# Performance work log

Measured on AMD Instinct MI355X. Metric: run time of the kernel, lower is better.

## Reference

```python
import jax, jax.numpy as jnp
import numpy as np

K = 20          # neighbors per centroid
OUT_CH = 256    # out_channel
EPS = 1e-5      # batchnorm eps


def _bn(x, gamma, beta, axes):
    # batch-norm in training mode (batch statistics), per-channel on last axis
    mu = jnp.mean(x, axis=axes, keepdims=True)
    var = jnp.var(x, axis=axes, keepdims=True)
    return (x - mu) * jax.lax.rsqrt(var + EPS) * gamma + beta


def _forward(centroid, xyz, radius, dist,
             w_xyz, b_xyz, g0, be0, w1, g1, be1, w2, g2, be2):
    B, N, _ = xyz.shape
    M = centroid.shape[1]
    # --- sample_and_group: radius mask + index sort + gather ---
    ar = jnp.arange(N, dtype=jnp.int32)                       # [N]
    idx = jnp.where(dist > radius, N, ar[None, None, :])      # [B,M,N]
    idx = jnp.sort(idx, axis=-1)[:, :, :K]                    # [B,M,K] lowest in-radius indices
    first = idx[:, :, :1]
    idx = jnp.where(idx == N, first, idx)                     # pad with first neighbor
    pf = jax.vmap(lambda f, i: f[i])(xyz, idx)                # [B,M,K,3] gather
    # --- concat (points, neighbors, variance) -> 9 channels ---
    pts = jnp.broadcast_to(centroid[:, :, None, :], (B, M, K, 3))
    feat = jnp.concatenate([pts, pf, pf - pts], axis=-1)      # [B,M,K,9]
    # --- 1x1 conv2d + BN2d + GELU (exact erf, as torch nn.GELU) ---
    h = jnp.einsum('bmkc,oc->bmko', feat, w_xyz) + b_xyz      # [B,M,K,C/8]
    h = jax.nn.gelu(_bn(h, g0, be0, axes=(0, 1, 2)), approximate=False)
    # --- max over k neighbors ---
    h = jnp.max(h, axis=2)                                    # [B,M,C/8]
    # --- MLP: Conv1x1 (no bias) + BN1d + GELU, then Conv1x1 + BN1d ---
    h = jnp.einsum('bmc,oc->bmo', h, w1)
    h = jax.nn.gelu(_bn(h, g1, be1, axes=(0, 1)), approximate=False)
    h = jnp.einsum('bmc,oc->bmo', h, w2)
    h = _bn(h, g2, be2, axes=(0, 1))                          # [B,M,OUT_CH]
    return h


def setup_inputs() -> dict:
    key = jax.random.key(0)
    ks = jax.random.split(key, 10)
    B, M, N = 4, 2048, 8192
    c8, c4 = OUT_CH // 8, OUT_CH // 4
    return {
        'centroid': jax.random.uniform(ks[0], (B, M, 3), jnp.float32),
        'xyz': jax.random.uniform(ks[1], (B, N, 3), jnp.float32),
        'radius': jax.random.uniform(ks[2], (B, M, 1), jnp.float32),
        'dist': jax.random.uniform(ks[3], (B, M, N), jnp.float32),
        'w_xyz': jax.random.normal(ks[4], (c8, 9), jnp.float32) * 0.3,
        'b_xyz': jnp.zeros((c8,), jnp.float32),
        'g0': jnp.ones((c8,), jnp.float32),
        'be0': jnp.zeros((c8,), jnp.float32),
        'w1': jax.random.normal(ks[5], (c4, c8), jnp.float32) * 0.2,
        'g1': jnp.ones((c4,), jnp.float32),
        'be1': jnp.zeros((c4,), jnp.float32),
        'w2': jax.random.normal(ks[6], (OUT_CH, c4), jnp.float32) * 0.15,
        'g2': jnp.ones((OUT_CH,), jnp.float32),
        'be2': jnp.zeros((OUT_CH,), jnp.float32),
    }


def reference(centroid, xyz, radius, dist, w_xyz, b_xyz, g0, be0,
              w1, g1, be1, w2, g2, be2):
    return _forward(centroid, xyz, radius, dist, w_xyz, b_xyz, g0, be0,
                    w1, g1, be1, w2, g2, be2)
```

## Files before the change

### kernel.cpp

```cpp
#include <hip/hip_runtime.h>
#include <cstdint>
#include <cstddef>

#define K_NB   20
#define N_PTS  8192
#define M_CENT 2048
#define B_SZ   4
#define C8     32
#define C4     64
#define COUT   256
#define EPSV   1e-5f
#define NROWS  (B_SZ * M_CENT)

#define NP0 64
#define NP1 32
#define NP2 16

__device__ __forceinline__ float gelu_exact(float x) {
    return 0.5f * x * (1.0f + erff(x * 0.7071067811865476f));
}

__global__ __launch_bounds__(256) void k_scan_mlp0(
    const float* __restrict__ centroid, const float* __restrict__ xyz,
    const float* __restrict__ radius,   const float* __restrict__ dist,
    const float* __restrict__ w_xyz,    const float* __restrict__ b_xyz,
    float* __restrict__ hmin, float* __restrict__ hmax,
    double* __restrict__ p0sum, double* __restrict__ p0sq)
{
    __shared__ int   idx_sh[4][K_NB];
    __shared__ float ss[256], qq[256];
    const int tid  = threadIdx.x;
    const int wave = tid >> 6;
    const int lane = tid & 63;
    const int row  = blockIdx.x * 4 + wave;
    const int b    = row >> 11;
    const float rad = radius[row];
    const float* drow = dist + (size_t)row * N_PTS;

    int cnt = 0;
    for (int base = 0; base < N_PTS && cnt < K_NB; base += 1024) {
        float4 v[4];
        #pragma unroll
        for (int s = 0; s < 4; s++)
            v[s] = reinterpret_cast<const float4*>(drow + base + s * 256)[lane];
        #pragma unroll
        for (int s = 0; s < 4; s++) {
            unsigned mloc = (v[s].x <= rad ? 1u : 0u) | (v[s].y <= rad ? 2u : 0u)
                          | (v[s].z <= rad ? 4u : 0u) | (v[s].w <= rad ? 8u : 0u);
            uint64_t b0 = __ballot(mloc & 1u);
            uint64_t b1 = __ballot(mloc & 2u);
            uint64_t b2 = __ballot(mloc & 4u);
            uint64_t b3 = __ballot(mloc & 8u);
            uint64_t lt = (1ull << lane) - 1ull;
            int r = __popcll(b0 & lt) + __popcll(b1 & lt)
                  + __popcll(b2 & lt) + __popcll(b3 & lt);
            const int myidx = base + s * 256 + lane * 4;
            if (mloc & 1u) { int p = cnt + r; if (p < K_NB) idx_sh[wave][p] = myidx + 0; r++; }
            if (mloc & 2u) { int p = cnt + r; if (p < K_NB) idx_sh[wave][p] = myidx + 1; r++; }
            if (mloc & 4u) { int p = cnt + r; if (p < K_NB) idx_sh[wave][p] = myidx + 2; r++; }
            if (mloc & 8u) { int p = cnt + r; if (p < K_NB) idx_sh[wave][p] = myidx + 3; r++; }
            cnt += __popcll(b0) + __popcll(b1) + __popcll(b2) + __popcll(b3);
        }
    }
    __syncthreads();

    const int cfill = (cnt < K_NB) ? cnt : K_NB;
    const int fillv = (cnt == 0) ? (N_PTS - 1) : idx_sh[wave][0];
    if (lane < K_NB && lane >= cfill) idx_sh[wave][lane] = fillv;
    __syncthreads();

    const int ch = lane & 31;
    const int kk = lane >> 5;
    const float* w = w_xyz + ch * 9;
    const float wc0 = w[0] - w[6], wc1 = w[1] - w[7], wc2 = w[2] - w[8];
    const float wp0 = w[3] + w[6], wp1 = w[4] + w[7], wp2 = w[5] + w[8];
    const float cterm = b_xyz[ch] + centroid[row * 3 + 0] * wc0
                      + centroid[row * 3 + 1] * wc1
                      + centroid[row * 3 + 2] * wc2;

    float s = 0.f, q = 0.f, mn = 3.0e38f, mx = -3.0e38f;
    #pragma unroll
    for (int t = 0; t < 10; t++) {
        const int idx = idx_sh[wave][2 * t + kk];
        const float* p = xyz + ((size_t)b * N_PTS + idx) * 3;
        const float h = cterm + p[0] * wp0 + p[1] * wp1 + p[2] * wp2;
        s += h; q += h * h;
        mn = fminf(mn, h); mx = fmaxf(mx, h);
    }
    mn = fminf(mn, __shfl_xor(mn, 32));
    mx = fmaxf(mx, __shfl_xor(mx, 32));
    if (lane < 32) hmin[row * C8 + ch] = mn;
    else           hmax[row * C8 + ch] = mx;

    ss[tid] = s; qq[tid] = q;
    __syncthreads();
    if (tid < C8) {
        float S = 0.f, Q = 0.f;
        #pragma unroll
        for (int r = 0; r < 8; r++) { S += ss[tid + 32 * r]; Q += qq[tid + 32 * r]; }
        const int part = blockIdx.x & (NP0 - 1);
        atomicAdd(&p0sum[part * C8 + tid], (double)S);
        atomicAdd(&p0sq [part * C8 + tid], (double)Q);
    }
}

__global__ __launch_bounds__(256) void k_bn0_max_mm1(
    const float* __restrict__ hmin, const float* __restrict__ hmax,
    const double* __restrict__ p0sum, const double* __restrict__ p0sq,
    const float* __restrict__ g0, const float* __restrict__ be0,
    const float* __restrict__ w1, float* __restrict__ h1,
    double* __restrict__ p1sum, double* __restrict__ p1sq)
{
    __shared__ float sc[C8], sh[C8];
    __shared__ float w1s[C4 * C8];
    __shared__ float a_sh[4][C8];
    __shared__ float r1s[4][C4];
    const int tid = threadIdx.x;
    if (tid < C8) {
        double S = 0.0, Q = 0.0;
        #pragma unroll 8
        for (int p = 0; p < NP0; p++) { S += p0sum[p * C8 + tid]; Q += p0sq[p * C8 + tid]; }
        const double inv = 1.0 / (double)((long)NROWS * K_NB);
        const double mu  = S * inv;
        const double var = Q * inv - mu * mu;
        const float sf = g0[tid] / sqrtf((float)var + EPSV);
        sc[tid] = sf;
        sh[tid] = be0[tid] - (float)mu * sf;
    }
    for (int i = tid; i < C4 * C8; i += 256) w1s[i] = w1[i];
    __syncthreads();

    const int wave = tid >> 6, lane = tid & 63;
    const int row  = blockIdx.x * 4 + wave;
    const int ch   = lane & 31;
    const float v  = (lane < 32 ? hmin : hmax)[row * C8 + ch];
    float ge = gelu_exact(v * sc[ch] + sh[ch]);
    ge = fmaxf(ge, __shfl_xor(ge, 32));
    if (lane < 32) a_sh[wave][lane] = ge;
    __syncthreads();

    float acc = 0.f;
    #pragma unroll
    for (int c = 0; c < C8; c++) acc += a_sh[wave][c] * w1s[lane * C8 + c];
    h1[(size_t)row * C4 + lane] = acc;

    r1s[wave][lane] = acc;
    __syncthreads();
    if (tid < C4) {
        const float v0 = r1s[0][tid], v1 = r1s[1][tid], v2 = r1s[2][tid], v3 = r1s[3][tid];
        const float S = v0 + v1 + v2 + v3;
        const float Q = v0 * v0 + v1 * v1 + v2 * v2 + v3 * v3;
        const int part = blockIdx.x & (NP1 - 1);
        atomicAdd(&p1sum[part * C4 + tid], (double)S);
        atomicAdd(&p1sq [part * C4 + tid], (double)Q);
    }
}

__global__ __launch_bounds__(256) void k_bn1_mm2(
    const float* __restrict__ h1,
    const double* __restrict__ p1sum, const double* __restrict__ p1sq,
    const float* __restrict__ g1, const float* __restrict__ be1,
    const float* __restrict__ w2, float* __restrict__ h2,
    double* __restrict__ p2sum, double* __restrict__ p2sq)
{
    __shared__ float sc[C4], sh[C4];
    __shared__ float a_sh[4][C4];
    __shared__ float v2s[4][COUT];
    const int tid = threadIdx.x;
    if (tid < C4) {
        double S = 0.0, Q = 0.0;
        #pragma unroll 8
        for (int p = 0; p < NP1; p++) { S += p1sum[p * C4 + tid]; Q += p1sq[p * C4 + tid]; }
        const double inv = 1.0 / (double)NROWS;
        const double mu  = S * inv;
        const double var = Q * inv - mu * mu;
        const float sf = g1[tid] / sqrtf((float)var + EPSV);
        sc[tid] = sf;
        sh[tid] = be1[tid] - (float)mu * sf;
    }
    __syncthreads();

    const int wave = tid >> 6, lane = tid & 63;
    const int row  = blockIdx.x * 4 + wave;
    const float v  = h1[(size_t)row * C4 + lane];
    a_sh[wave][lane] = gelu_exact(v * sc[lane] + sh[lane]);
    __syncthreads();

    float acc0 = 0.f, acc1 = 0.f, acc2 = 0.f, acc3 = 0.f;
    #pragma unroll 8
    for (int c = 0; c < C4; c++) {
        const float a = a_sh[wave][c];
        acc0 += a * w2[(0 * 64 + lane) * C4 + c];
        acc1 += a * w2[(1 * 64 + lane) * C4 + c];
        acc2 += a * w2[(2 * 64 + lane) * C4 + c];
        acc3 += a * w2[(3 * 64 + lane) * C4 + c];
    }
    float* orow = h2 + (size_t)row * COUT;
    orow[0 * 64 + lane] = acc0;
    orow[1 * 64 + lane] = acc1;
    orow[2 * 64 + lane] = acc2;
    orow[3 * 64 + lane] = acc3;

    v2s[wave][0 * 64 + lane] = acc0;
    v2s[wave][1 * 64 + lane] = acc1;
    v2s[wave][2 * 64 + lane] = acc2;
    v2s[wave][3 * 64 + lane] = acc3;
    __syncthreads();
    {
        float S = 0.f, Q = 0.f;
        #pragma unroll
        for (int w = 0; w < 4; w++) { const float x = v2s[w][tid]; S += x; Q += x * x; }
        const int part = blockIdx.x & (NP2 - 1);
        atomicAdd(&p2sum[part * COUT + tid], (double)S);
        atomicAdd(&p2sq [part * COUT + tid], (double)Q);
    }
}

__global__ __launch_bounds__(256) void k_bn2_out(
    const float* __restrict__ h2,
    const double* __restrict__ p2sum, const double* __restrict__ p2sq,
    const float* __restrict__ g2, const float* __restrict__ be2,
    float* __restrict__ out)
{
    __shared__ float sc[COUT], sh[COUT];
    const int tid = threadIdx.x;
    {
        double S = 0.0, Q = 0.0;
        #pragma unroll
        for (int p = 0; p < NP2; p++) { S += p2sum[p * COUT + tid]; Q += p2sq[p * COUT + tid]; }
        const double inv = 1.0 / (double)NROWS;
        const double mu  = S * inv;
        const double var = Q * inv - mu * mu;
        const float sf = g2[tid] / sqrtf((float)var + EPSV);
        sc[tid] = sf;
        sh[tid] = be2[tid] - (float)mu * sf;
    }
    __syncthreads();
    const int total4 = NROWS * COUT / 4;
    for (int i = blockIdx.x * 256 + tid; i < total4; i += gridDim.x * 256) {
        const float4 v = reinterpret_cast<const float4*>(h2)[i];
        const int ch = (i * 4) & 255;
        float4 o;
        o.x = v.x * sc[ch + 0] + sh[ch + 0];
        o.y = v.y * sc[ch + 1] + sh[ch + 1];
        o.z = v.z * sc[ch + 2] + sh[ch + 2];
        o.w = v.w * sc[ch + 3] + sh[ch + 3];
        reinterpret_cast<float4*>(out)[i] = o;
    }
}

extern "C" void kernel_launch(void* const* d_in, const int* in_sizes, int n_in,
                              void* d_out, int out_size, void* d_ws, size_t ws_size,
                              hipStream_t stream) {
    const float* centroid = (const float*)d_in[0];
    const float* xyz      = (const float*)d_in[1];
    const float* radius   = (const float*)d_in[2];
    const float* dist     = (const float*)d_in[3];
    const float* w_xyz    = (const float*)d_in[4];
    const float* b_xyz    = (const float*)d_in[5];
    const float* g0       = (const float*)d_in[6];
    const float* be0      = (const float*)d_in[7];
    const float* w1       = (const float*)d_in[8];
    const float* g1       = (const float*)d_in[9];
    const float* be1      = (const float*)d_in[10];
    const float* w2       = (const float*)d_in[11];
    const float* g2       = (const float*)d_in[12];
    const float* be2      = (const float*)d_in[13];
    float* out = (float*)d_out;

    char* ws = (char*)d_ws;
    double* p0sum = (double*)ws;
    double* p0sq  = p0sum + NP0 * C8;
    double* p1sum = p0sq  + NP0 * C8;
    double* p1sq  = p1sum + NP1 * C4;
    double* p2sum = p1sq  + NP1 * C4;
    double* p2sq  = p2sum + NP2 * COUT;
    float* hmin = (float*)(ws + 131072);
    float* hmax = hmin + (size_t)NROWS * C8;
    float* h1   = hmax + (size_t)NROWS * C8;
    float* h2   = h1   + (size_t)NROWS * C4;

    k_scan_mlp0<<<NROWS / 4, 256, 0, stream>>>(centroid, xyz, radius, dist,
                                               w_xyz, b_xyz, hmin, hmax,
                                               p0sum, p0sq);
    k_bn0_max_mm1<<<NROWS / 4, 256, 0, stream>>>(hmin, hmax, p0sum, p0sq,
                                                 g0, be0, w1, h1, p1sum, p1sq);
    k_bn1_mm2<<<NROWS / 4, 256, 0, stream>>>(h1, p1sum, p1sq, g1, be1, w2,
                                             h2, p2sum, p2sq);
    k_bn2_out<<<512, 256, 0, stream>>>(h2, p2sum, p2sq, g2, be2, out);
}
```

Baseline: 421.0 us.

## Fuse all four stages into one cooperative kernel with grid syncs

Replaces the four separate kernels with a single cooperative kernel of 512 blocks. Each wave now processes 4 rows, and grid.sync() separates the BN statistic phases. Intermediates (hmin/hmax, h1, h2) stay in registers and shared memory instead of round-tripping through global memory, and three launches go away. The cost is three grid-wide barriers, a dependence on cooperative launch residency, and less parallelism during the latency-bound dist scan because each wave handles its 4 rows one after another.

```diff
diff --git a/kernel.cpp b/kernel.cpp
--- a/kernel.cpp
+++ b/kernel.cpp
@@ -1,121 +1,134 @@
 #include <hip/hip_runtime.h>
+#include <hip/hip_cooperative_groups.h>
 #include <cstdint>
 #include <cstddef>
 
+namespace cg = cooperative_groups;
+
 #define K_NB   20
 #define N_PTS  8192
-#define M_CENT 2048
-#define B_SZ   4
 #define C8     32
 #define C4     64
 #define COUT   256
 #define EPSV   1e-5f
-#define NROWS  (B_SZ * M_CENT)
-
-#define NP0 64
-#define NP1 32
-#define NP2 16
+#define NROWS  8192
+#define NBLK   512
+#define RPW    4
+#define NP0    16
+#define NP1    16
+#define NP2    16
 
 __device__ __forceinline__ float gelu_exact(float x) {
     return 0.5f * x * (1.0f + erff(x * 0.7071067811865476f));
 }
 
-__global__ __launch_bounds__(256) void k_scan_mlp0(
+__global__ __launch_bounds__(256, 4) void k_fused(
     const float* __restrict__ centroid, const float* __restrict__ xyz,
     const float* __restrict__ radius,   const float* __restrict__ dist,
     const float* __restrict__ w_xyz,    const float* __restrict__ b_xyz,
-    float* __restrict__ hmin, float* __restrict__ hmax,
-    double* __restrict__ p0sum, double* __restrict__ p0sq)
+    const float* __restrict__ g0,  const float* __restrict__ be0,
+    const float* __restrict__ w1,  const float* __restrict__ g1,
+    const float* __restrict__ be1, const float* __restrict__ w2,
+    const float* __restrict__ g2,  const float* __restrict__ be2,
+    float* __restrict__ out,
+    double* __restrict__ p0sum, double* __restrict__ p0sq,
+    double* __restrict__ p1sum, double* __restrict__ p1sq,
+    double* __restrict__ p2sum, double* __restrict__ p2sq)
 {
+    cg::grid_group grid = cg::this_grid();
+
     __shared__ int   idx_sh[4][K_NB];
     __shared__ float ss[256], qq[256];
+    __shared__ float sc0[C8],  sh0[C8];
+    __shared__ float w1t[C8 * C4];
+    __shared__ float a_sh[4][RPW][C8];
+    __shared__ float sc1[C4],  sh1[C4];
+    __shared__ float a1_sh[4][RPW][C4];
+    __shared__ float s2s[4][COUT], q2s[4][COUT];
+    __shared__ float sc2[COUT], sh2[COUT];
+
     const int tid  = threadIdx.x;
     const int wave = tid >> 6;
     const int lane = tid & 63;
-    const int row  = blockIdx.x * 4 + wave;
-    const int b    = row >> 11;
-    const float rad = radius[row];
-    const float* drow = dist + (size_t)row * N_PTS;
-
-    int cnt = 0;
-    for (int base = 0; base < N_PTS && cnt < K_NB; base += 1024) {
-        float4 v[4];
-        #pragma unroll
-        for (int s = 0; s < 4; s++)
-            v[s] = reinterpret_cast<const float4*>(drow + base + s * 256)[lane];
-        #pragma unroll
-        for (int s = 0; s < 4; s++) {
-            unsigned mloc = (v[s].x <= rad ? 1u : 0u) | (v[s].y <= rad ? 2u : 0u)
-                          | (v[s].z <= rad ? 4u : 0u) | (v[s].w <= rad ? 8u : 0u);
-            uint64_t b0 = __ballot(mloc & 1u);
-            uint64_t b1 = __ballot(mloc & 2u);
-            uint64_t b2 = __ballot(mloc & 4u);
-            uint64_t b3 = __ballot(mloc & 8u);
-            uint64_t lt = (1ull << lane) - 1ull;
-            int r = __popcll(b0 & lt) + __popcll(b1 & lt)
-                  + __popcll(b2 & lt) + __popcll(b3 & lt);
-            const int myidx = base + s * 256 + lane * 4;
-            if (mloc & 1u) { int p = cnt + r; if (p < K_NB) idx_sh[wave][p] = myidx + 0; r++; }
-            if (mloc & 2u) { int p = cnt + r; if (p < K_NB) idx_sh[wave][p] = myidx + 1; r++; }
-            if (mloc & 4u) { int p = cnt + r; if (p < K_NB) idx_sh[wave][p] = myidx + 2; r++; }
-            if (mloc & 8u) { int p = cnt + r; if (p < K_NB) idx_sh[wave][p] = myidx + 3; r++; }
-            cnt += __popcll(b0) + __popcll(b1) + __popcll(b2) + __popcll(b3);
-        }
-    }
-    __syncthreads();
-
-    const int cfill = (cnt < K_NB) ? cnt : K_NB;
-    const int fillv = (cnt == 0) ? (N_PTS - 1) : idx_sh[wave][0];
-    if (lane < K_NB && lane >= cfill) idx_sh[wave][lane] = fillv;
-    __syncthreads();
-
-    const int ch = lane & 31;
-    const int kk = lane >> 5;
-    const float* w = w_xyz + ch * 9;
-    const float wc0 = w[0] - w[6], wc1 = w[1] - w[7], wc2 = w[2] - w[8];
-    const float wp0 = w[3] + w[6], wp1 = w[4] + w[7], wp2 = w[5] + w[8];
-    const float cterm = b_xyz[ch] + centroid[row * 3 + 0] * wc0
-                      + centroid[row * 3 + 1] * wc1
-                      + centroid[row * 3 + 2] * wc2;
-
-    float s = 0.f, q = 0.f, mn = 3.0e38f, mx = -3.0e38f;
-    #pragma unroll
-    for (int t = 0; t < 10; t++) {
-        const int idx = idx_sh[wave][2 * t + kk];
-        const float* p = xyz + ((size_t)b * N_PTS + idx) * 3;
-        const float h = cterm + p[0] * wp0 + p[1] * wp1 + p[2] * wp2;
-        s += h; q += h * h;
-        mn = fminf(mn, h); mx = fmaxf(mx, h);
-    }
-    mn = fminf(mn, __shfl_xor(mn, 32));
-    mx = fmaxf(mx, __shfl_xor(mx, 32));
-    if (lane < 32) hmin[row * C8 + ch] = mn;
-    else           hmax[row * C8 + ch] = mx;
-
-    ss[tid] = s; qq[tid] = q;
+    const int gw   = blockIdx.x * 4 + wave;
+    const int ch   = lane & 31;
+    const int kk   = lane >> 5;
+
+    const float* wr = w_xyz + ch * 9;
+    const float wc0 = wr[0] - wr[6], wc1 = wr[1] - wr[7], wc2 = wr[2] - wr[8];
+    const float wp0 = wr[3] + wr[6], wp1 = wr[4] + wr[7], wp2 = wr[5] + wr[8];
+    const float bch = b_xyz[ch];
+
+    float e[RPW];
+    float s_acc = 0.f, q_acc = 0.f;
+
+    for (int r = 0; r < RPW; ++r) {
+        const int row = gw * RPW + r;
+        const int b   = row >> 11;
+        const float rad = radius[row];
+        const float* drow = dist + (size_t)row * N_PTS;
+
+        int cnt = 0;
+        for (int base = 0; base < N_PTS && cnt < K_NB; base += 1024) {
+            float4 v[4];
+            #pragma unroll
+            for (int s = 0; s < 4; s++)
+                v[s] = reinterpret_cast<const float4*>(drow + base + s * 256)[lane];
+            #pragma unroll
+            for (int s = 0; s < 4; s++) {
+                unsigned mloc = (v[s].x <= rad ? 1u : 0u) | (v[s].y <= rad ? 2u : 0u)
+                              | (v[s].z <= rad ? 4u : 0u) | (v[s].w <= rad ? 8u : 0u);
+                uint64_t b0 = __ballot(mloc & 1u);
+                uint64_t b1 = __ballot(mloc & 2u);
+                uint64_t b2 = __ballot(mloc & 4u);
+                uint64_t b3 = __ballot(mloc & 8u);
+                uint64_t lt = (1ull << lane) - 1ull;
+                int rk = __popcll(b0 & lt) + __popcll(b1 & lt)
+                       + __popcll(b2 & lt) + __popcll(b3 & lt);
+                const int myidx = base + s * 256 + lane * 4;
+                if (mloc & 1u) { int p = cnt + rk; if (p < K_NB) idx_sh[wave][p] = myidx + 0; rk++; }
+                if (mloc & 2u) { int p = cnt + rk; if (p < K_NB) idx_sh[wave][p] = myidx + 1; rk++; }
+                if (mloc & 4u) { int p = cnt + rk; if (p < K_NB) idx_sh[wave][p] = myidx + 2; rk++; }
+                if (mloc & 8u) { int p = cnt + rk; if (p < K_NB) idx_sh[wave][p] = myidx + 3; rk++; }
+                cnt += __popcll(b0) + __popcll(b1) + __popcll(b2) + __popcll(b3);
+            }
+        }
+        __syncthreads();
+        const int cfill = (cnt < K_NB) ? cnt : K_NB;
+        const int fillv = (cnt == 0) ? (N_PTS - 1) : idx_sh[wave][0];
+        if (lane < K_NB && lane >= cfill) idx_sh[wave][lane] = fillv;
+        __syncthreads();
+
+        const float cterm = bch + centroid[row * 3 + 0] * wc0
+                          + centroid[row * 3 + 1] * wc1
+                          + centroid[row * 3 + 2] * wc2;
+        float s = 0.f, q = 0.f, mn = 3.0e38f, mx = -3.0e38f;
+        #pragma unroll
+        for (int t = 0; t < 10; t++) {
+            const int idx = idx_sh[wave][2 * t + kk];
+            const float* p = xyz + ((size_t)b * N_PTS + idx) * 3;
+            const float h = cterm + p[0] * wp0 + p[1] * wp1 + p[2] * wp2;
+            s += h; q += h * h;
+            mn = fminf(mn, h); mx = fmaxf(mx, h);
+        }
+        s_acc += s; q_acc += q;
+        mn = fminf(mn, __shfl_xor(mn, 32));
+        mx = fmaxf(mx, __shfl_xor(mx, 32));
+        e[r] = (lane < 32) ? mn : mx;
+    }
+
+    ss[tid] = s_acc; qq[tid] = q_acc;
     __syncthreads();
     if (tid < C8) {
         float S = 0.f, Q = 0.f;
         #pragma unroll
-        for (int r = 0; r < 8; r++) { S += ss[tid + 32 * r]; Q += qq[tid + 32 * r]; }
+        for (int rr = 0; rr < 8; rr++) { S += ss[tid + 32 * rr]; Q += qq[tid + 32 * rr]; }
         const int part = blockIdx.x & (NP0 - 1);
         atomicAdd(&p0sum[part * C8 + tid], (double)S);
         atomicAdd(&p0sq [part * C8 + tid], (double)Q);
     }
-}
-
-__global__ __launch_bounds__(256) void k_bn0_max_mm1(
-    const float* __restrict__ hmin, const float* __restrict__ hmax,
-    const double* __restrict__ p0sum, const double* __restrict__ p0sq,
-    const float* __restrict__ g0, const float* __restrict__ be0,
-    const float* __restrict__ w1, float* __restrict__ h1,
-    double* __restrict__ p1sum, double* __restrict__ p1sq)
-{
-    __shared__ float sc[C8], sh[C8];
-    __shared__ float w1s[C4 * C8];
-    __shared__ float a_sh[4][C8];
-    __shared__ float r1s[4][C4];
-    const int tid = threadIdx.x;
+    grid.sync();
+
     if (tid < C8) {
         double S = 0.0, Q = 0.0;
         #pragma unroll 8
@@ -124,49 +137,47 @@
         const double mu  = S * inv;
         const double var = Q * inv - mu * mu;
         const float sf = g0[tid] / sqrtf((float)var + EPSV);
-        sc[tid] = sf;
-        sh[tid] = be0[tid] - (float)mu * sf;
-    }
-    for (int i = tid; i < C4 * C8; i += 256) w1s[i] = w1[i];
-    __syncthreads();
-
-    const int wave = tid >> 6, lane = tid & 63;
-    const int row  = blockIdx.x * 4 + wave;
-    const int ch   = lane & 31;
-    const float v  = (lane < 32 ? hmin : hmax)[row * C8 + ch];
-    float ge = gelu_exact(v * sc[ch] + sh[ch]);
-    ge = fmaxf(ge, __shfl_xor(ge, 32));
-    if (lane < 32) a_sh[wave][lane] = ge;
-    __syncthreads();
-
-    float acc = 0.f;
-    #pragma unroll
-    for (int c = 0; c < C8; c++) acc += a_sh[wave][c] * w1s[lane * C8 + c];
-    h1[(size_t)row * C4 + lane] = acc;
-
-    r1s[wave][lane] = acc;
+        sc0[tid] = sf;
+        sh0[tid] = be0[tid] - (float)mu * sf;
+    }
+    for (int i = tid; i < C4 * C8; i += 256) {
+        const int o = i >> 5, c = i & 31;
+        w1t[c * C4 + o] = w1[i];
+    }
+    __syncthreads();
+
+    #pragma unroll
+    for (int r = 0; r < RPW; ++r) {
+        float g = gelu_exact(e[r] * sc0[ch] + sh0[ch]);
+        g = fmaxf(g, __shfl_xor(g, 32));
+        if (lane < 32) a_sh[wave][r][lane] = g;
+    }
+    __syncthreads();
+
+    float h1r[RPW];
+    #pragma unroll
+    for (int r = 0; r < RPW; ++r) {
+        float acc = 0.f;
+        #pragma unroll
+        for (int c = 0; c < C8; c++) acc += a_sh[wave][r][c] * w1t[c * C4 + lane];
+        h1r[r] = acc;
+    }
+    {
+        float S = 0.f, Q = 0.f;
+        #pragma unroll
+        for (int r = 0; r < RPW; ++r) { S += h1r[r]; Q += h1r[r] * h1r[r]; }
+        ss[tid] = S; qq[tid] = Q;
+    }
     __syncthreads();
     if (tid < C4) {
-        const float v0 = r1s[0][tid], v1 = r1s[1][tid], v2 = r1s[2][tid], v3 = r1s[3][tid];
-        const float S = v0 + v1 + v2 + v3;
-        const float Q = v0 * v0 + v1 * v1 + v2 * v2 + v3 * v3;
+        const float S = ss[tid] + ss[tid + 64] + ss[tid + 128] + ss[tid + 192];
+        const float Q = qq[tid] + qq[tid + 64] + qq[tid + 128] + qq[tid + 192];
         const int part = blockIdx.x & (NP1 - 1);
         atomicAdd(&p1sum[part * C4 + tid], (double)S);
         atomicAdd(&p1sq [part * C4 + tid], (double)Q);
     }
-}
-
-__global__ __launch_bounds__(256) void k_bn1_mm2(
-    const float* __restrict__ h1,
-    const double* __restrict__ p1sum, const double* __restrict__ p1sq,
-    const float* __restrict__ g1, const float* __restrict__ be1,
-    const float* __restrict__ w2, float* __restrict__ h2,
-    double* __restrict__ p2sum, double* __restrict__ p2sq)
-{
-    __shared__ float sc[C4], sh[C4];
-    __shared__ float a_sh[4][C4];
-    __shared__ float v2s[4][COUT];
-    const int tid = threadIdx.x;
+    grid.sync();
+
     if (tid < C4) {
         double S = 0.0, Q = 0.0;
         #pragma unroll 8
@@ -175,77 +186,67 @@
         const double mu  = S * inv;
         const double var = Q * inv - mu * mu;
         const float sf = g1[tid] / sqrtf((float)var + EPSV);
-        sc[tid] = sf;
-        sh[tid] = be1[tid] - (float)mu * sf;
-    }
-    __syncthreads();
-
-    const int wave = tid >> 6, lane = tid & 63;
-    const int row  = blockIdx.x * 4 + wave;
-    const float v  = h1[(size_t)row * C4 + lane];
-    a_sh[wave][lane] = gelu_exact(v * sc[lane] + sh[lane]);
-    __syncthreads();
-
-    float acc0 = 0.f, acc1 = 0.f, acc2 = 0.f, acc3 = 0.f;
-    #pragma unroll 8
-    for (int c = 0; c < C4; c++) {
-        const float a = a_sh[wave][c];
-        acc0 += a * w2[(0 * 64 + lane) * C4 + c];
-        acc1 += a * w2[(1 * 64 + lane) * C4 + c];
-        acc2 += a * w2[(2 * 64 + lane) * C4 + c];
-        acc3 += a * w2[(3 * 64 + lane) * C4 + c];
-    }
-    float* orow = h2 + (size_t)row * COUT;
-    orow[0 * 64 + lane] = acc0;
-    orow[1 * 64 + lane] = acc1;
-    orow[2 * 64 + lane] = acc2;
-    orow[3 * 64 + lane] = acc3;
-
-    v2s[wave][0 * 64 + lane] = acc0;
-    v2s[wave][1 * 64 + lane] = acc1;
-    v2s[wave][2 * 64 + lane] = acc2;
-    v2s[wave][3 * 64 + lane] = acc3;
+        sc1[tid] = sf;
+        sh1[tid] = be1[tid] - (float)mu * sf;
+    }
+    __syncthreads();
+    #pragma unroll
+    for (int r = 0; r < RPW; ++r)
+        a1_sh[wave][r][lane] = gelu_exact(h1r[r] * sc1[lane] + sh1[lane]);
+    __syncthreads();
+
+    float acc[RPW][4] = {};
+    #pragma unroll 4
+    for (int c = 0; c < C4; ++c) {
+        float av[RPW];
+        #pragma unroll
+        for (int r = 0; r < RPW; ++r) av[r] = a1_sh[wave][r][c];
+        #pragma unroll
+        for (int j = 0; j < 4; j++) {
+            const float wv = w2[(j * 64 + lane) * C4 + c];
+            #pragma unroll
+            for (int r = 0; r < RPW; ++r) acc[r][j] += av[r] * wv;
+        }
+    }
+    #pragma unroll
+    for (int j = 0; j < 4; j++) {
+        float S = 0.f, Q = 0.f;
+        #pragma unroll
+        for (int r = 0; r < RPW; ++r) { S += acc[r][j]; Q += acc[r][j] * acc[r][j]; }
+        s2s[wave][j * 64 + lane] = S;
+        q2s[wave][j * 64 + lane] = Q;
+    }
     __syncthreads();
     {
-        float S = 0.f, Q = 0.f;
-        #pragma unroll
-        for (int w = 0; w < 4; w++) { const float x = v2s[w][tid]; S += x; Q += x * x; }
+        const float S = s2s[0][tid] + s2s[1][tid] + s2s[2][tid] + s2s[3][tid];
+        const float Q = q2s[0][tid] + q2s[1][tid] + q2s[2][tid] + q2s[3][tid];
         const int part = blockIdx.x & (NP2 - 1);
         atomicAdd(&p2sum[part * COUT + tid], (double)S);
         atomicAdd(&p2sq [part * COUT + tid], (double)Q);
     }
-}
-
-__global__ __launch_bounds__(256) void k_bn2_out(
-    const float* __restrict__ h2,
-    const double* __restrict__ p2sum, const double* __restrict__ p2sq,
-    const float* __restrict__ g2, const float* __restrict__ be2,
-    float* __restrict__ out)
-{
-    __shared__ float sc[COUT], sh[COUT];
-    const int tid = threadIdx.x;
+    grid.sync();
+
     {
         double S = 0.0, Q = 0.0;
-        #pragma unroll
+        #pragma unroll 8
         for (int p = 0; p < NP2; p++) { S += p2sum[p * COUT + tid]; Q += p2sq[p * COUT + tid]; }
         const double inv = 1.0 / (double)NROWS;
         const double mu  = S * inv;
         const double var = Q * inv - mu * mu;
         const float sf = g2[tid] / sqrtf((float)var + EPSV);
-        sc[tid] = sf;
-        sh[tid] = be2[tid] - (float)mu * sf;
-    }
-    __syncthreads();
-    const int total4 = NROWS * COUT / 4;
-    for (int i = blockIdx.x * 256 + tid; i < total4; i += gridDim.x * 256) {
-        const float4 v = reinterpret_cast<const float4*>(h2)[i];
-        const int ch = (i * 4) & 255;
-        float4 o;
-        o.x = v.x * sc[ch + 0] + sh[ch + 0];
-        o.y = v.y * sc[ch + 1] + sh[ch + 1];
-        o.z = v.z * sc[ch + 2] + sh[ch + 2];
-        o.w = v.w * sc[ch + 3] + sh[ch + 3];
-        reinterpret_cast<float4*>(out)[i] = o;
+        sc2[tid] = sf;
+        sh2[tid] = be2[tid] - (float)mu * sf;
+    }
+    __syncthreads();
+    #pragma unroll
+    for (int r = 0; r < RPW; ++r) {
+        const int row = gw * RPW + r;
+        float* orow = out + (size_t)row * COUT;
+        #pragma unroll
+        for (int j = 0; j < 4; j++) {
+            const int oc = j * 64 + lane;
+            orow[oc] = acc[r][j] * sc2[oc] + sh2[oc];
+        }
     }
 }
 
@@ -275,17 +276,15 @@
     double* p1sq  = p1sum + NP1 * C4;
     double* p2sum = p1sq  + NP1 * C4;
     double* p2sq  = p2sum + NP2 * COUT;
-    float* hmin = (float*)(ws + 131072);
-    float* hmax = hmin + (size_t)NROWS * C8;
-    float* h1   = hmax + (size_t)NROWS * C8;
-    float* h2   = h1   + (size_t)NROWS * C4;
-
-    k_scan_mlp0<<<NROWS / 4, 256, 0, stream>>>(centroid, xyz, radius, dist,
-                                               w_xyz, b_xyz, hmin, hmax,
-                                               p0sum, p0sq);
-    k_bn0_max_mm1<<<NROWS / 4, 256, 0, stream>>>(hmin, hmax, p0sum, p0sq,
-                                                 g0, be0, w1, h1, p1sum, p1sq);
-    k_bn1_mm2<<<NROWS / 4, 256, 0, stream>>>(h1, p1sum, p1sq, g1, be1, w2,
-                                             h2, p2sum, p2sq);
-    k_bn2_out<<<512, 256, 0, stream>>>(h2, p2sum, p2sq, g2, be2, out);
+
+    void* args[] = {
+        (void*)&centroid, (void*)&xyz, (void*)&radius, (void*)&dist,
+        (void*)&w_xyz, (void*)&b_xyz, (void*)&g0, (void*)&be0,
+        (void*)&w1, (void*)&g1, (void*)&be1, (void*)&w2, (void*)&g2, (void*)&be2,
+        (void*)&out,
+        (void*)&p0sum, (void*)&p0sq, (void*)&p1sum, (void*)&p1sq,
+        (void*)&p2sum, (void*)&p2sq };
+
+    hipLaunchCooperativeKernel((const void*)k_fused, dim3(NBLK), dim3(256),
+                               args, 0, stream);
 }
```

Measured after the change: 539.8 us. 28.2% more time.
